# Kernel tuning notes

Hardware: AMD Instinct MI355X
Metric: run time of the kernel (lower is better)

The kernel has to match this reference:

```python
import jax, jax.numpy as jnp
import numpy as np

TAU_PRE = 2.0   # pre-synaptic trace time constant
SCALE = 1.0     # forward(scale=1.0) default
SPIKE_P = 0.1   # firing probability for realistic binary spike trains


def setup_inputs() -> dict:
    key = jax.random.key(0)
    k1, k2 = jax.random.split(key)
    T, B, NIN, NOUT = 2048, 128, 256, 128
    # binary spike trains, [T, B, N]
    in_spikes = (jax.random.uniform(k1, (T, B, NIN)) < SPIKE_P).astype(jnp.float32)
    out_spikes = (jax.random.uniform(k2, (T, B, NOUT)) < SPIKE_P).astype(jnp.float32)
    return {"in_spikes": in_spikes, "out_spikes": out_spikes}


def reference(in_spikes, out_spikes):
    # STDP.forward: loop over recorded timesteps, per step:
    #   trace_pre = trace_pre - trace_pre/tau_pre + in_spike          (decayed trace)
    #   dw = sum_b trace_pre[b, :] (outer) out_spike[b, :] -> [NOUT, NIN]
    #   delta_w += scale * dw
    # Expressed as a single lax.scan over the time axis.
    B, NIN = in_spikes.shape[1], in_spikes.shape[2]
    NOUT = out_spikes.shape[2]

    def step(carry, xs):
        trace_pre, delta_w = carry
        s_in, s_out = xs                                 # [B, NIN], [B, NOUT]
        trace_pre = trace_pre - trace_pre / TAU_PRE + s_in
        dw = jnp.einsum('bi,bo->oi', trace_pre, s_out)   # [NOUT, NIN]
        return (trace_pre, delta_w + SCALE * dw), None

    init = (jnp.zeros((B, NIN), in_spikes.dtype),
            jnp.zeros((NOUT, NIN), in_spikes.dtype))
    (_, delta_w), _ = jax.lax.scan(step, init, (in_spikes, out_spikes))
    return delta_w
```

## Files before the change

### kernel.cpp

```cpp
#include <hip/hip_runtime.h>
#include <hip/hip_bf16.h>

#define T_TOTAL 2048
#define BATCH   128
#define NIN     256
#define NOUT    128

#define TC      512
#define NTC     (T_TOTAL / TC)
#define BC      2
#define NBP     (BATCH / BC)
#define NBLOCKS (NBP * NTC)
#define WARM    32
#define CT      8
#define NCH     (TC / CT)

#define STRI    (BATCH * NIN)
#define STRO    (BATCH * NOUT)
#define OUT_ELEMS (NOUT * NIN)

typedef __attribute__((ext_vector_type(8)))  __bf16 bf16x8;
typedef __attribute__((ext_vector_type(2)))  __bf16 bf16x2;
typedef __attribute__((ext_vector_type(16))) float  f32x16;

static __device__ __forceinline__ unsigned pack_bf16(float a, float b) {
    bf16x2 v = { (__bf16)a, (__bf16)b };
    union { bf16x2 v; unsigned u; } c; c.v = v; return c.u;
}
static __device__ __forceinline__ bf16x8 frag4(unsigned w0, unsigned w1,
                                               unsigned w2, unsigned w3) {
    union { unsigned u[4]; bf16x8 f; } c;
    c.u[0] = w0; c.u[1] = w1; c.u[2] = w2; c.u[3] = w3; return c.f;
}

__global__ __launch_bounds__(1024, 4)
void stdp_main(const float* __restrict__ in, const float* __restrict__ outs,
               float* __restrict__ dst, int use_atomic)
{
    const int tid  = threadIdx.x;
    const int lane = tid & 63;
    const int l31  = lane & 31;
    const int kh   = lane >> 5;
    const int wv   = tid >> 6;
    const int nt   = wv & 7;
    const int mh   = wv >> 3;

    const int tc = blockIdx.x & 3;
    const int bp = blockIdx.x >> 2;
    const int b0 = bp * BC;
    const int t0 = tc * TC;

    const size_t in_off = (size_t)(b0 + kh) * NIN + nt * 32 + l31;
    const size_t ot_off = (size_t)(b0 + kh) * NOUT + mh * 64 + l31;

    float tr = 0.f;

    if (tc > 0) {
        for (int t = t0 - WARM; t < t0; t += 8) {
            float v[8];
#pragma unroll
            for (int u = 0; u < 8; ++u) v[u] = in[(size_t)(t + u) * STRI + in_off];
#pragma unroll
            for (int u = 0; u < 8; ++u) tr = 0.5f * tr + v[u];
        }
    }

    f32x16 acc[2];
    acc[0] = (f32x16)(0.f);
    acc[1] = (f32x16)(0.f);

    float cin[2][8];
    float af[2][2][8];

#pragma unroll
    for (int j = 0; j < 8; ++j) cin[0][j] = in[(size_t)(t0 + j) * STRI + in_off];
#pragma unroll
    for (int mm = 0; mm < 2; ++mm)
#pragma unroll
        for (int j = 0; j < 8; ++j)
            af[0][mm][j] = outs[(size_t)(t0 + j) * STRO + ot_off + mm * 32];

    auto body = [&](int cur, int c) {
        const int tb  = t0 + c * CT;
        const int nxt = cur ^ 1;

        if (c + 1 < NCH) {
#pragma unroll
            for (int j = 0; j < 8; ++j)
                cin[nxt][j] = in[(size_t)(tb + CT + j) * STRI + in_off];
#pragma unroll
            for (int mm = 0; mm < 2; ++mm)
#pragma unroll
                for (int j = 0; j < 8; ++j)
                    af[nxt][mm][j] = outs[(size_t)(tb + CT + j) * STRO + ot_off + mm * 32];
        }

        unsigned bw[4];
#pragma unroll
        for (int p = 0; p < 4; ++p) {
            tr = 0.5f * tr + cin[cur][2 * p];
            const float f0 = tr;
            tr = 0.5f * tr + cin[cur][2 * p + 1];
            bw[p] = pack_bf16(f0, tr);
        }
        const bf16x8 bfrag = frag4(bw[0], bw[1], bw[2], bw[3]);

#pragma unroll
        for (int mm = 0; mm < 2; ++mm) {
            const bf16x8 afrag = frag4(pack_bf16(af[cur][mm][0], af[cur][mm][1]),
                                       pack_bf16(af[cur][mm][2], af[cur][mm][3]),
                                       pack_bf16(af[cur][mm][4], af[cur][mm][5]),
                                       pack_bf16(af[cur][mm][6], af[cur][mm][7]));
            acc[mm] = __builtin_amdgcn_mfma_f32_32x32x16_bf16(afrag, bfrag, acc[mm], 0, 0, 0);
        }
    };

    for (int cc = 0; cc < NCH; cc += 2) {
        body(0, cc);
        body(1, cc + 1);
    }

    const int icol = nt * 32 + l31;
    if (use_atomic) {
#pragma unroll
        for (int mm = 0; mm < 2; ++mm)
#pragma unroll
            for (int r = 0; r < 16; ++r) {
                const int row = (r & 3) + 8 * (r >> 2) + 4 * kh;
                const int o   = mh * 64 + mm * 32 + row;
                atomicAdd(&dst[o * NIN + icol], acc[mm][r]);
            }
    } else {
        float* base = dst + (size_t)blockIdx.x * OUT_ELEMS;
#pragma unroll
        for (int mm = 0; mm < 2; ++mm)
#pragma unroll
            for (int r = 0; r < 16; ++r) {
                const int row = (r & 3) + 8 * (r >> 2) + 4 * kh;
                const int o   = mh * 64 + mm * 32 + row;
                base[o * NIN + icol] = acc[mm][r];
            }
    }
}

__global__ void zero_kernel(float* p, int n) {
    int i = blockIdx.x * blockDim.x + threadIdx.x;
    if (i < n) p[i] = 0.f;
}

__global__ __launch_bounds__(256)
void reduce_kernel(const float* __restrict__ ws, float* __restrict__ outp) {
    const int idx = blockIdx.x * 256 + threadIdx.x;
    float s = 0.f;
    for (int k = 0; k < NBLOCKS; k += 16) {
        float v[16];
#pragma unroll
        for (int u = 0; u < 16; ++u) v[u] = ws[(size_t)(k + u) * OUT_ELEMS + idx];
#pragma unroll
        for (int u = 0; u < 16; ++u) s += v[u];
    }
    outp[idx] = s;
}

extern "C" void kernel_launch(void* const* d_in, const int* in_sizes, int n_in,
                              void* d_out, int out_size, void* d_ws, size_t ws_size,
                              hipStream_t stream) {
    const float* in   = (const float*)d_in[0];
    const float* outs = (const float*)d_in[1];
    float* out = (float*)d_out;
    float* ws  = (float*)d_ws;

    if (ws_size >= (size_t)NBLOCKS * OUT_ELEMS * sizeof(float)) {
        stdp_main<<<NBLOCKS, 1024, 0, stream>>>(in, outs, ws, 0);
        reduce_kernel<<<OUT_ELEMS / 256, 256, 0, stream>>>(ws, out);
    } else {
        zero_kernel<<<(OUT_ELEMS + 255) / 256, 256, 0, stream>>>(out, OUT_ELEMS);
        stdp_main<<<NBLOCKS, 1024, 0, stream>>>(in, outs, out, 1);
    }
}
```

Measured before the change: 477.5 us.

## Reformulate STDP as backward post-trace scan with binary input operand and prefetch pump

Rewrites the accumulation using the identity sum_t trace_pre(t) x out(t) = sum_t in(t) x R(t), where R is a reverse-time decayed sum of output spikes. The scan now runs backward over outputs, so the binary input spikes go straight into the MFMA B operand via a cheap bit-truncation pack instead of a bf16 convert. Warp tiling changes so each wave owns one 32-row output tile and two input tiles, with the trace computed on outputs instead of inputs. Volatile 'pump' loads replace the register double buffer as a cache prefetch two chunks ahead, which adds extra memory traffic and drops the explicit software pipelining.

```diff
diff --git a/kernel.cpp b/kernel.cpp
--- a/kernel.cpp
+++ b/kernel.cpp
@@ -8,8 +8,7 @@
 
 #define TC      512
 #define NTC     (T_TOTAL / TC)
-#define BC      2
-#define NBP     (BATCH / BC)
+#define NBP     (BATCH / 2)
 #define NBLOCKS (NBP * NTC)
 #define WARM    32
 #define CT      8
@@ -22,10 +21,14 @@
 typedef __attribute__((ext_vector_type(8)))  __bf16 bf16x8;
 typedef __attribute__((ext_vector_type(2)))  __bf16 bf16x2;
 typedef __attribute__((ext_vector_type(16))) float  f32x16;
+typedef __attribute__((ext_vector_type(4)))  float  f32x4;
 
 static __device__ __forceinline__ unsigned pack_bf16(float a, float b) {
     bf16x2 v = { (__bf16)a, (__bf16)b };
     union { bf16x2 v; unsigned u; } c; c.v = v; return c.u;
+}
+static __device__ __forceinline__ unsigned pack_bin(float a, float b) {
+    return (__float_as_uint(a) >> 16) | (__float_as_uint(b) & 0xFFFF0000u);
 }
 static __device__ __forceinline__ bf16x8 frag4(unsigned w0, unsigned w1,
                                                unsigned w2, unsigned w3) {
@@ -42,26 +45,39 @@
     const int l31  = lane & 31;
     const int kh   = lane >> 5;
     const int wv   = tid >> 6;
-    const int nt   = wv & 7;
-    const int mh   = wv >> 3;
+    const int mt   = wv & 3;
+    const int ng   = wv >> 2;
 
     const int tc = blockIdx.x & 3;
     const int bp = blockIdx.x >> 2;
-    const int b0 = bp * BC;
-    const int t0 = tc * TC;
+    const int b0 = bp * 2;
+    const int t_hi = (tc + 1) * TC;
 
-    const size_t in_off = (size_t)(b0 + kh) * NIN + nt * 32 + l31;
-    const size_t ot_off = (size_t)(b0 + kh) * NOUT + mh * 64 + l31;
+    const size_t ot_ch  = (size_t)(b0 + kh) * NOUT + mt * 32 + l31;
+    const size_t in_off = (size_t)(b0 + kh) * NIN;
 
-    float tr = 0.f;
+    const int pj = wv & 7, pd = wv >> 3;
 
-    if (tc > 0) {
-        for (int t = t0 - WARM; t < t0; t += 8) {
+    auto pump = [&](int tp) {
+        volatile const f32x4* p1 = (volatile const f32x4*)
+            &in[(size_t)(tp + pj) * STRI + (size_t)(b0 + pd) * NIN + lane * 4];
+        f32x4 x = *p1; (void)x;
+        if (pd) {
+            volatile const f32x4* p2 = (volatile const f32x4*)
+                &outs[(size_t)(tp + pj) * STRO + (size_t)b0 * NOUT + lane * 4];
+            f32x4 y = *p2; (void)y;
+        }
+    };
+
+    float r = 0.f;
+
+    if (tc < NTC - 1) {
+        for (int t = t_hi + WARM - 8; t >= t_hi; t -= 8) {
             float v[8];
 #pragma unroll
-            for (int u = 0; u < 8; ++u) v[u] = in[(size_t)(t + u) * STRI + in_off];
+            for (int u = 0; u < 8; ++u) v[u] = outs[(size_t)(t + u) * STRO + ot_ch];
 #pragma unroll
-            for (int u = 0; u < 8; ++u) tr = 0.5f * tr + v[u];
+            for (int u = 7; u >= 0; --u) r = v[u] + 0.5f * r;
         }
     }
 
@@ -69,77 +85,63 @@
     acc[0] = (f32x16)(0.f);
     acc[1] = (f32x16)(0.f);
 
-    float cin[2][8];
-    float af[2][2][8];
+    pump(t_hi - CT);
+    pump(t_hi - 2 * CT);
 
+    for (int c = 0; c < NCH; ++c) {
+        const int tb = t_hi - (c + 1) * CT;
+
+        if (c + 2 < NCH) pump(tb - 2 * CT);
+
+        float ov[8];
 #pragma unroll
-    for (int j = 0; j < 8; ++j) cin[0][j] = in[(size_t)(t0 + j) * STRI + in_off];
+        for (int j = 0; j < 8; ++j) ov[j] = outs[(size_t)(tb + j) * STRO + ot_ch];
+
+        float bv[2][8];
 #pragma unroll
-    for (int mm = 0; mm < 2; ++mm)
+        for (int n = 0; n < 2; ++n) {
+            const size_t io = in_off + (ng * 2 + n) * 32 + l31;
 #pragma unroll
-        for (int j = 0; j < 8; ++j)
-            af[0][mm][j] = outs[(size_t)(t0 + j) * STRO + ot_off + mm * 32];
-
-    auto body = [&](int cur, int c) {
-        const int tb  = t0 + c * CT;
-        const int nxt = cur ^ 1;
-
-        if (c + 1 < NCH) {
-#pragma unroll
-            for (int j = 0; j < 8; ++j)
-                cin[nxt][j] = in[(size_t)(tb + CT + j) * STRI + in_off];
-#pragma unroll
-            for (int mm = 0; mm < 2; ++mm)
-#pragma unroll
-                for (int j = 0; j < 8; ++j)
-                    af[nxt][mm][j] = outs[(size_t)(tb + CT + j) * STRO + ot_off + mm * 32];
+            for (int j = 0; j < 8; ++j) bv[n][j] = in[(size_t)(tb + j) * STRI + io];
         }
 
-        unsigned bw[4];
+        float rr[8];
 #pragma unroll
-        for (int p = 0; p < 4; ++p) {
-            tr = 0.5f * tr + cin[cur][2 * p];
-            const float f0 = tr;
-            tr = 0.5f * tr + cin[cur][2 * p + 1];
-            bw[p] = pack_bf16(f0, tr);
+        for (int j = 7; j >= 0; --j) { r = ov[j] + 0.5f * r; rr[j] = r; }
+
+        const bf16x8 afrag = frag4(pack_bf16(rr[0], rr[1]), pack_bf16(rr[2], rr[3]),
+                                   pack_bf16(rr[4], rr[5]), pack_bf16(rr[6], rr[7]));
+#pragma unroll
+        for (int n = 0; n < 2; ++n) {
+            const bf16x8 bfrag = frag4(pack_bin(bv[n][0], bv[n][1]),
+                                       pack_bin(bv[n][2], bv[n][3]),
+                                       pack_bin(bv[n][4], bv[n][5]),
+                                       pack_bin(bv[n][6], bv[n][7]));
+            acc[n] = __builtin_amdgcn_mfma_f32_32x32x16_bf16(afrag, bfrag, acc[n], 0, 0, 0);
         }
-        const bf16x8 bfrag = frag4(bw[0], bw[1], bw[2], bw[3]);
-
-#pragma unroll
-        for (int mm = 0; mm < 2; ++mm) {
-            const bf16x8 afrag = frag4(pack_bf16(af[cur][mm][0], af[cur][mm][1]),
-                                       pack_bf16(af[cur][mm][2], af[cur][mm][3]),
-                                       pack_bf16(af[cur][mm][4], af[cur][mm][5]),
-                                       pack_bf16(af[cur][mm][6], af[cur][mm][7]));
-            acc[mm] = __builtin_amdgcn_mfma_f32_32x32x16_bf16(afrag, bfrag, acc[mm], 0, 0, 0);
-        }
-    };
-
-    for (int cc = 0; cc < NCH; cc += 2) {
-        body(0, cc);
-        body(1, cc + 1);
     }
 
-    const int icol = nt * 32 + l31;
     if (use_atomic) {
 #pragma unroll
-        for (int mm = 0; mm < 2; ++mm)
+        for (int n = 0; n < 2; ++n) {
+            const int icol = (ng * 2 + n) * 32 + l31;
 #pragma unroll
-            for (int r = 0; r < 16; ++r) {
-                const int row = (r & 3) + 8 * (r >> 2) + 4 * kh;
-                const int o   = mh * 64 + mm * 32 + row;
-                atomicAdd(&dst[o * NIN + icol], acc[mm][r]);
+            for (int q = 0; q < 16; ++q) {
+                const int row = (q & 3) + 8 * (q >> 2) + 4 * kh;
+                atomicAdd(&dst[(mt * 32 + row) * NIN + icol], acc[n][q]);
             }
+        }
     } else {
         float* base = dst + (size_t)blockIdx.x * OUT_ELEMS;
 #pragma unroll
-        for (int mm = 0; mm < 2; ++mm)
+        for (int n = 0; n < 2; ++n) {
+            const int icol = (ng * 2 + n) * 32 + l31;
 #pragma unroll
-            for (int r = 0; r < 16; ++r) {
-                const int row = (r & 3) + 8 * (r >> 2) + 4 * kh;
-                const int o   = mh * 64 + mm * 32 + row;
-                base[o * NIN + icol] = acc[mm][r];
+            for (int q = 0; q < 16; ++q) {
+                const int row = (q & 3) + 8 * (q >> 2) + 4 * kh;
+                base[(mt * 32 + row) * NIN + icol] = acc[n][q];
             }
+        }
     }
 }
 
```

Measured after the change: 497.4 us. +4.2%, slower.
